# Optimization experiments

Measured on AMD Instinct MI355X. Metric: run time of the kernel, lower is better.

## Reference

```python
import jax, jax.numpy as jnp
import numpy as np

N = 10000      # nodes
E = 160000     # edges (before self-loops)
IN = 256
NEG_SLOPE = 0.2  # PyG GATConv default


def gat_layer(x, src, dst, W, a_src, a_dst, bias, heads, concat, n):
    # x: [n, in_dim]; W: [in_dim, heads*C]; a_src/a_dst: [heads, C]
    C = W.shape[1] // heads
    h = (x @ W).reshape(n, heads, C)                      # [n,H,C]
    es = jnp.einsum('nhc,hc->nh', h, a_src)               # [n,H]
    ed = jnp.einsum('nhc,hc->nh', h, a_dst)               # [n,H]
    e = jax.nn.leaky_relu(es[src] + ed[dst], NEG_SLOPE)   # [E,H]
    # segment softmax over destination node (every node has a self-loop)
    emax = jax.ops.segment_max(e, dst, num_segments=n)    # [n,H]
    al = jnp.exp(e - emax[dst])                           # [E,H]
    den = jax.ops.segment_sum(al, dst, num_segments=n)    # [n,H]
    al = al / den[dst]
    out = jax.ops.segment_sum(h[src] * al[:, :, None], dst, num_segments=n)  # [n,H,C]
    out = out.reshape(n, heads * C) if concat else out.mean(axis=1)
    return out + bias


def setup_inputs() -> dict:
    key = jax.random.key(0)
    ks = jax.random.split(key, 16)
    s = 0.05
    p = lambda k, shp: jax.random.normal(k, shp, dtype=jnp.float32) * s
    return {
        'x': jax.random.normal(ks[0], (N, IN), dtype=jnp.float32),
        'edge_index': jax.random.randint(ks[1], (2, E), 0, N, dtype=jnp.int64),
        'proj_w': p(ks[2], (IN, 512)), 'proj_b': jnp.zeros((512,), jnp.float32),
        'w1': p(ks[3], (512, 4 * 512)),  'as1': p(ks[4], (4, 512)), 'ad1': p(ks[5], (4, 512)),  'b1': jnp.zeros((2048,), jnp.float32),
        'w2': p(ks[6], (2048, 4 * 512)), 'as2': p(ks[7], (4, 512)), 'ad2': p(ks[8], (4, 512)),  'b2': jnp.zeros((2048,), jnp.float32),
        'w3': p(ks[9], (2048, 2 * 512)), 'as3': p(ks[10], (2, 512)), 'ad3': p(ks[11], (2, 512)), 'b3': jnp.zeros((512,), jnp.float32),
    }


def reference(x, edge_index, proj_w, proj_b, w1, as1, ad1, b1,
              w2, as2, ad2, b2, w3, as3, ad3, b3):
    n = x.shape[0]
    loops = jnp.arange(n, dtype=edge_index.dtype)
    src = jnp.concatenate([edge_index[0], loops])   # PyG add_self_loops=True
    dst = jnp.concatenate([edge_index[1], loops])
    h = x @ proj_w + proj_b                         # dropout is identity in eval
    h = gat_layer(h, src, dst, w1, as1, ad1, b1, 4, True, n)
    h = jax.nn.elu(h)
    h = gat_layer(h, src, dst, w2, as2, ad2, b2, 4, True, n)
    h = jax.nn.elu(h)
    h = gat_layer(h, src, dst, w3, as3, ad3, b3, 2, False, n)
    return h
```

## Files before the change

### kernel.cpp

```cpp
#include <hip/hip_runtime.h>
#include <hip/hip_bf16.h>
#include <math.h>

#define CDIV(a,b) (((a)+(b)-1)/(b))

typedef __bf16  bf16x8 __attribute__((ext_vector_type(8)));
typedef float   f32x4  __attribute__((ext_vector_type(4)));
typedef unsigned short u16x8 __attribute__((ext_vector_type(8)));
typedef unsigned short u16x4 __attribute__((ext_vector_type(4)));

__device__ __forceinline__ float bf2f(unsigned short u) {
    union { unsigned int i; float f; } x; x.i = ((unsigned int)u) << 16; return x.f;
}
__device__ __forceinline__ unsigned short f2bf(float f) {
    union { float f; unsigned int i; } x; x.f = f;
    unsigned int r = x.i + 0x7fff + ((x.i >> 16) & 1);
    return (unsigned short)(r >> 16);
}

__global__ void hist_kernel(const int* __restrict__ ei, int* __restrict__ deg,
                            int E, int Et) {
    int e = blockIdx.x * blockDim.x + threadIdx.x;
    if (e >= Et) return;
    int d = (e < E) ? ei[E + e] : (e - E);
    atomicAdd(&deg[d], 1);
}

__global__ void scan_kernel(const int* __restrict__ deg, int* __restrict__ off, int n) {
    __shared__ int wsum[16];
    __shared__ int carry_s;
    int t = threadIdx.x, lane = t & 63, wv = t >> 6;
    if (t == 0) carry_s = 0;
    __syncthreads();
    for (int base = 0; base < n; base += 1024) {
        int v = (base + t < n) ? deg[base + t] : 0;
        int x = v;
#pragma unroll
        for (int o = 1; o < 64; o <<= 1) {
            int y = __shfl_up(x, o);
            if (lane >= o) x += y;
        }
        if (lane == 63) wsum[wv] = x;
        __syncthreads();
        if (wv == 0 && lane < 16) {
            int s = wsum[lane];
#pragma unroll
            for (int o = 1; o < 16; o <<= 1) {
                int y = __shfl_up(s, o);
                if (lane >= o) s += y;
            }
            wsum[lane] = s;
        }
        __syncthreads();
        int wprev = (wv == 0) ? 0 : wsum[wv - 1];
        int incl = carry_s + wprev + x;
        if (base + t < n) off[base + t] = incl - v;
        __syncthreads();
        if (t == 1023) carry_s = incl;
        __syncthreads();
    }
    if (t == 0) off[n] = carry_s;
}

__global__ void scatter_kernel(const int* __restrict__ ei, const int* __restrict__ off,
                               int* __restrict__ cur, int* __restrict__ csr,
                               int E, int Et) {
    int e = blockIdx.x * blockDim.x + threadIdx.x;
    if (e >= Et) return;
    int s, d;
    if (e < E) { s = ei[e]; d = ei[E + e]; } else { s = e - E; d = s; }
    int pos = off[d] + atomicAdd(&cur[d], 1);
    csr[pos] = s;
}

__global__ void prep_t_kernel(const float* __restrict__ wa, __hip_bfloat16* __restrict__ wta,
                              const float* __restrict__ wb, __hip_bfloat16* __restrict__ wtb,
                              const float* __restrict__ wc, __hip_bfloat16* __restrict__ wtc,
                              int t0, int t1, int t2) {
    __shared__ float tile[32][33];
    int bid = blockIdx.x;
    const float* w; __hip_bfloat16* wt; int K, N, r;
    if (bid < t0)      { w = wa; wt = wta; K = 512;  N = 2048; r = bid; }
    else if (bid < t1) { w = wb; wt = wtb; K = 2048; N = 2048; r = bid - t0; }
    else               { w = wc; wt = wtc; K = 2048; N = 1024; r = bid - t1; }
    (void)t2;
    int kt = K >> 5;
    int kb = (r % kt) * 32, nb = (r / kt) * 32;
    int tx = threadIdx.x & 31, ty = threadIdx.x >> 5;
    for (int i = ty; i < 32; i += 8)
        tile[i][tx] = w[(size_t)(kb + i) * N + nb + tx];
    __syncthreads();
    for (int i = ty; i < 32; i += 8)
        wt[(size_t)(nb + i) * K + kb + tx] = __float2bfloat16(tile[tx][i]);
}

__global__ void cvt2_kernel(const float* __restrict__ a, __hip_bfloat16* __restrict__ ao,
                            int na4,
                            const float* __restrict__ b, __hip_bfloat16* __restrict__ bo,
                            int nb4) {
    int i = blockIdx.x * blockDim.x + threadIdx.x;
    const float* src; __hip_bfloat16* dst; int idx;
    if (i < na4) { src = a; dst = ao; idx = i * 4; }
    else if (i < na4 + nb4) { src = b; dst = bo; idx = (i - na4) * 4; }
    else return;
    float4 v = *(const float4*)(src + idx);
    dst[idx + 0] = __float2bfloat16(v.x);
    dst[idx + 1] = __float2bfloat16(v.y);
    dst[idx + 2] = __float2bfloat16(v.z);
    dst[idx + 3] = __float2bfloat16(v.w);
}

__global__ void beff_kernel(const float* __restrict__ pb, const float* __restrict__ w1,
                            float* __restrict__ beff, int N) {
    int j  = blockIdx.x * 256 + threadIdx.x;
    int k0 = blockIdx.y * 64;
    float s = 0.f;
#pragma unroll
    for (int k = 0; k < 64; k++)
        s = fmaf(pb[k0 + k], w1[(size_t)(k0 + k) * N + j], s);
    atomicAdd(&beff[j], s);
}

__global__ void va_kernel(const __hip_bfloat16* __restrict__ w_efft,
                          const float* __restrict__ b_eff,
                          const float* __restrict__ as1, const float* __restrict__ ad1,
                          const float* __restrict__ b1,
                          float* __restrict__ va, float* __restrict__ cvec,
                          float* __restrict__ b1s) {
    int j = blockIdx.x, t = threadIdx.x;
    if (j == 8) {
        for (int i = t; i < 2048; i += 256) b1s[i] = b_eff[i] + b1[i];
        return;
    }
    int h = j & 3;
    const float* a = ((j < 4) ? as1 : ad1) + h * 512;
    __shared__ float aLDS[512];
    __shared__ float red[256];
    for (int c = t; c < 512; c += 256) aLDS[c] = a[c];
    __syncthreads();
    float acc = 0.f;
    const unsigned short* wb = (const unsigned short*)w_efft + (size_t)h * 512 * 256 + t;
    for (int c = 0; c < 512; c++)
        acc = fmaf(aLDS[c], bf2f(wb[(size_t)c * 256]), acc);
    va[j * 256 + t] = acc;
    float cp = b_eff[h * 512 + t] * aLDS[t] + b_eff[h * 512 + 256 + t] * aLDS[256 + t];
    red[t] = cp;
    __syncthreads();
    for (int s = 128; s > 0; s >>= 1) {
        if (t < s) red[t] += red[t + s];
        __syncthreads();
    }
    if (t == 0) cvec[j] = red[0];
}

__global__ void es1_kernel(const __hip_bfloat16* __restrict__ x_bf,
                           const float* __restrict__ va, const float* __restrict__ cvec,
                           float* __restrict__ es, float* __restrict__ ed) {
    int node = blockIdx.x, l = threadIdx.x;
    u16x4 xv = *(const u16x4*)((const unsigned short*)x_bf + (size_t)node * 256 + l * 4);
    float xf[4];
#pragma unroll
    for (int k = 0; k < 4; k++) xf[k] = bf2f(xv[k]);
    float dot[8];
#pragma unroll
    for (int j = 0; j < 8; j++) {
        float4 v = *(const float4*)(va + j * 256 + l * 4);
        dot[j] = xf[0] * v.x + xf[1] * v.y + xf[2] * v.z + xf[3] * v.w;
    }
#pragma unroll
    for (int j = 0; j < 8; j++)
        for (int o = 32; o; o >>= 1) dot[j] += __shfl_down(dot[j], o);
    if (l == 0) {
#pragma unroll
        for (int h = 0; h < 4; h++) {
            es[node * 4 + h] = dot[h] + cvec[h];
            ed[node * 4 + h] = dot[4 + h] + cvec[4 + h];
        }
    }
}

__global__ __launch_bounds__(256) void agg1x_kernel(
    const __hip_bfloat16* __restrict__ x_bf, const float* __restrict__ es,
    const float* __restrict__ ed, const int* __restrict__ csr,
    const int* __restrict__ off, __hip_bfloat16* __restrict__ z)
{
    __shared__ float alds[64][4];
    __shared__ int   slds[64];
    int d = blockIdx.x, t = threadIdx.x;
    int beg = off[d], end = off[d + 1];
    float acc[4] = {0.f, 0.f, 0.f, 0.f}, den[4] = {0.f, 0.f, 0.f, 0.f};
    float edd[4];
#pragma unroll
    for (int h = 0; h < 4; h++) edd[h] = ed[d * 4 + h];
    const unsigned short* xb = (const unsigned short*)x_bf;

    for (int cb = beg; cb < end; cb += 64) {
        int cl = end - cb; if (cl > 64) cl = 64;
        int i = t >> 2, h = t & 3;
        if (i < cl) {
            int s = csr[cb + i];
            if (h == 0) slds[i] = s;
            float e = es[s * 4 + h] + edd[h];
            e = (e > 0.f) ? e : 0.2f * e;
            alds[i][h] = __expf(e);
        }
        __syncthreads();
        for (int ii = 0; ii < cl; ii++) {
            int s = slds[ii];
            float xv = bf2f(xb[(size_t)s * 256 + t]);
#pragma unroll
            for (int hh = 0; hh < 4; hh++) {
                float a = alds[ii][hh];
                den[hh] += a;
                acc[hh] = fmaf(a, xv, acc[hh]);
            }
        }
        __syncthreads();
    }
    unsigned short* zb = (unsigned short*)z + (size_t)d * 1024;
#pragma unroll
    for (int h = 0; h < 4; h++)
        zb[h * 256 + t] = f2bf(acc[h] / den[h]);
}

__device__ __forceinline__ void gload16(void* lds, const void* g) {
    __builtin_amdgcn_global_load_lds(
        (const __attribute__((address_space(1))) void*)g,
        (__attribute__((address_space(3))) void*)lds, 16, 0, 0);
}

__global__ __launch_bounds__(256) void gemm_bf16_kernel(
    const __hip_bfloat16* __restrict__ A,
    const __hip_bfloat16* __restrict__ BT,
    const float* __restrict__ bias,
    __hip_bfloat16* __restrict__ Cb,
    int M, int N, int K, int lda, int hko, int do_elu,
    int MB, int NB, int XT, int NBH)
{
    __shared__ __align__(16) __hip_bfloat16 As[128 * 32];
    __shared__ __align__(16) __hip_bfloat16 Bs[128 * 32];

    const int bid  = blockIdx.x;
    const int xcd  = bid & 7;
    const int slot = bid >> 3;
    const int per_yh = XT * NBH;
    const int yh    = slot / per_yh;
    const int rem   = slot - yh * per_yh;
    const int x_sub = rem / NBH;
    const int ys    = rem - x_sub * NBH;
    const int yb    = yh * NBH + ys;
    const int xb    = xcd * XT + x_sub;
    if (xb >= MB || yb >= NB) return;

    const int tid = threadIdx.x;
    const int m0 = xb * 128, n0 = yb * 128;
    const int w = tid >> 6, l = tid & 63;
    const int wm = (w & 1) * 64, wn = (w >> 1) * 64;
    const int lm = l & 15, lq = l >> 4;

    f32x4 acc[4][4] = {};

    const int arow = tid >> 2;
    const int acol = (tid & 3) * 8;
    const __hip_bfloat16* Ag = A + (size_t)(m0 + arow) * lda + acol + (n0 >> 9) * hko;
    const __hip_bfloat16* Bg = BT + (size_t)(n0 + arow) * K + acol;
    char* AsW = (char*)As + (w << 10);
    char* BsW = (char*)Bs + (w << 10);

    for (int k0 = 0; k0 < K; k0 += 32) {
        gload16(AsW,        Ag + k0);
        gload16(AsW + 4096, Ag + (size_t)64 * lda + k0);
        gload16(BsW,        Bg + k0);
        gload16(BsW + 4096, Bg + (size_t)64 * K + k0);
        __syncthreads();
        bf16x8 af[4], bfr[4];
#pragma unroll
        for (int i = 0; i < 4; i++)
            af[i] = *(const bf16x8*)(As + (wm + i * 16 + lm) * 32 + lq * 8);
#pragma unroll
        for (int j = 0; j < 4; j++)
            bfr[j] = *(const bf16x8*)(Bs + (wn + j * 16 + lm) * 32 + lq * 8);
#pragma unroll
        for (int i = 0; i < 4; i++)
#pragma unroll
            for (int j = 0; j < 4; j++)
                acc[i][j] = __builtin_amdgcn_mfma_f32_16x16x32_bf16(
                    af[i], bfr[j], acc[i][j], 0, 0, 0);
        __syncthreads();
    }

#pragma unroll
    for (int i = 0; i < 4; i++) {
        int rb = m0 + wm + i * 16 + lq * 4;
#pragma unroll
        for (int r = 0; r < 4; r++) {
            int row = rb + r;
            if (row >= M) continue;
#pragma unroll
            for (int j = 0; j < 4; j++) {
                int col = n0 + wn + j * 16 + lm;
                float v = acc[i][j][r];
                if (bias) v += bias[col];
                if (do_elu) v = (v > 0.f) ? v : expm1f(v);
                Cb[(size_t)row * N + col] = __float2bfloat16(v);
            }
        }
    }
}

__global__ __launch_bounds__(512, 2) void gemm256_kernel(
    const __hip_bfloat16* __restrict__ A,
    const __hip_bfloat16* __restrict__ BT,
    __hip_bfloat16* __restrict__ Cb,
    int M, int N, int K, int MT, int nfull)
{
    __shared__ __align__(16) char smem[131072];
    const int NT = K >> 6;

    const int cpx  = gridDim.x >> 3;
    const int bid  = blockIdx.x;
    const int slot = (bid & 7) * cpx + (bid >> 3);
    int mt, ntl;
    if (slot < nfull) { mt = slot % MT; ntl = slot / MT; }
    else              { ntl = nfull / MT; mt = (nfull % MT) + (slot - nfull); }
    const int m0 = mt << 8, n0 = ntl << 8;

    const int tid = threadIdx.x;
    const int w  = tid >> 6, l = tid & 63;
    const int wr = w >> 2, wc = w & 3;
    const int lm = l & 15, lq = l >> 4;

    const int srow = tid >> 3;
    const int scol = ((l & 7) << 3) ^ ((l >> 3) << 3);
    const __hip_bfloat16* As0 = A  + (size_t)(m0 + srow) * K + scol;
    const __hip_bfloat16* Bs0 = BT + (size_t)(n0 + srow) * K + scol;
    const size_t rs64  = (size_t)64  * K;
    const size_t rs128 = (size_t)128 * K;
    char* const stA = smem +          ((size_t)w << 10);
    char* const stB = smem + 65536 +  ((size_t)w << 10);

    auto STAGE_A = [&](int par, int hf, int tt) {
        char* d = stA + (((par << 1) | hf) << 14);
        const __hip_bfloat16* s = As0 + (size_t)hf * rs128 + (tt << 6);
        gload16(d,        s);
        gload16(d + 8192, s + rs64);
    };
    auto STAGE_B = [&](int par, int hf, int tt) {
        char* d = stB + (((par << 1) | hf) << 14);
        const __hip_bfloat16* s = Bs0 + (size_t)hf * rs128 + (tt << 6);
        gload16(d,        s);
        gload16(d + 8192, s + rs64);
    };

    const int roff = lm << 7;
    const int xm   = (lm & 7) << 4;
    const int off0 = (lq << 4) ^ xm;
    const int off1 = off0 ^ 64;
    const int bsel = 65536 + ((wc & 1) << 13);

    f32x4  acc[8][4] = {};
    bf16x8 af[8][2];
    bf16x8 bfr[2][2];

    STAGE_A(0, 0, 0); STAGE_A(0, 1, 0);
    STAGE_B(0, 0, 0); STAGE_B(0, 1, 0);
    STAGE_A(1, 0, 1); STAGE_A(1, 1, 1);
    asm volatile("s_waitcnt vmcnt(4)" ::: "memory");
    __builtin_amdgcn_s_barrier();

    for (int t = 0; t < NT; ++t) {
        const int par = t & 1;
        const char* aS = smem + (((par << 1) | wr)        << 14) + roff;
        const char* bS = smem + (((par << 1) | (wc >> 1)) << 14) + bsel + roff;

#pragma unroll
        for (int i = 0; i < 4; ++i) {
            af[i][0] = *(const bf16x8*)(aS + i * 2048 + off0);
            af[i][1] = *(const bf16x8*)(aS + i * 2048 + off1);
        }
#pragma unroll
        for (int j = 0; j < 2; ++j) {
            bfr[j][0] = *(const bf16x8*)(bS + j * 2048 + off0);
            bfr[j][1] = *(const bf16x8*)(bS + j * 2048 + off1);
        }
        if (t + 1 < NT) STAGE_B(par ^ 1, 0, t + 1);
        __builtin_amdgcn_s_barrier();
        asm volatile("s_waitcnt lgkmcnt(0)" ::: "memory");
        __builtin_amdgcn_sched_barrier(0);
        __builtin_amdgcn_s_setprio(1);
#pragma unroll
        for (int i = 0; i < 4; ++i)
#pragma unroll
            for (int j = 0; j < 2; ++j) {
                acc[i][j] = __builtin_amdgcn_mfma_f32_16x16x32_bf16(af[i][0], bfr[j][0], acc[i][j], 0, 0, 0);
                acc[i][j] = __builtin_amdgcn_mfma_f32_16x16x32_bf16(af[i][1], bfr[j][1], acc[i][j], 0, 0, 0);
            }
        __builtin_amdgcn_s_setprio(0);
        __builtin_amdgcn_s_barrier();

#pragma unroll
        for (int i = 4; i < 8; ++i) {
            af[i][0] = *(const bf16x8*)(aS + i * 2048 + off0);
            af[i][1] = *(const bf16x8*)(aS + i * 2048 + off1);
        }
        if (t + 1 < NT) STAGE_B(par ^ 1, 1, t + 1);
        __builtin_amdgcn_s_barrier();
        asm volatile("s_waitcnt lgkmcnt(0)" ::: "memory");
        __builtin_amdgcn_sched_barrier(0);
        __builtin_amdgcn_s_setprio(1);
#pragma unroll
        for (int i = 4; i < 8; ++i)
#pragma unroll
            for (int j = 0; j < 2; ++j) {
                acc[i][j] = __builtin_amdgcn_mfma_f32_16x16x32_bf16(af[i][0], bfr[j][0], acc[i][j], 0, 0, 0);
                acc[i][j] = __builtin_amdgcn_mfma_f32_16x16x32_bf16(af[i][1], bfr[j][1], acc[i][j], 0, 0, 0);
            }
        __builtin_amdgcn_s_setprio(0);
        __builtin_amdgcn_s_barrier();

#pragma unroll
        for (int j = 0; j < 2; ++j) {
            bfr[j][0] = *(const bf16x8*)(bS + (j + 2) * 2048 + off0);
            bfr[j][1] = *(const bf16x8*)(bS + (j + 2) * 2048 + off1);
        }
        if (t + 2 < NT) STAGE_A(par, 0, t + 2);
        __builtin_amdgcn_s_barrier();
        asm volatile("s_waitcnt lgkmcnt(0)" ::: "memory");
        __builtin_amdgcn_sched_barrier(0);
        __builtin_amdgcn_s_setprio(1);
#pragma unroll
        for (int i = 0; i < 4; ++i)
#pragma unroll
            for (int j = 0; j < 2; ++j) {
                acc[i][j + 2] = __builtin_amdgcn_mfma_f32_16x16x32_bf16(af[i][0], bfr[j][0], acc[i][j + 2], 0, 0, 0);
                acc[i][j + 2] = __builtin_amdgcn_mfma_f32_16x16x32_bf16(af[i][1], bfr[j][1], acc[i][j + 2], 0, 0, 0);
            }
        __builtin_amdgcn_s_setprio(0);
        __builtin_amdgcn_s_barrier();

        if (t + 2 < NT) STAGE_A(par, 1, t + 2);
        __builtin_amdgcn_s_barrier();
        __builtin_amdgcn_sched_barrier(0);
        __builtin_amdgcn_s_setprio(1);
#pragma unroll
        for (int i = 4; i < 8; ++i)
#pragma unroll
            for (int j = 0; j < 2; ++j) {
                acc[i][j + 2] = __builtin_amdgcn_mfma_f32_16x16x32_bf16(af[i][0], bfr[j][0], acc[i][j + 2], 0, 0, 0);
                acc[i][j + 2] = __builtin_amdgcn_mfma_f32_16x16x32_bf16(af[i][1], bfr[j][1], acc[i][j + 2], 0, 0, 0);
            }
        __builtin_amdgcn_s_setprio(0);
        if (t + 2 < NT)      { asm volatile("s_waitcnt vmcnt(4)" ::: "memory"); }
        else if (t + 1 < NT) { asm volatile("s_waitcnt vmcnt(0)" ::: "memory"); }
        __builtin_amdgcn_s_barrier();
    }

#pragma unroll
    for (int i = 0; i < 8; ++i) {
        int rb = m0 + wr * 128 + i * 16 + lq * 4;
#pragma unroll
        for (int r = 0; r < 4; ++r) {
            int row = rb + r;
            if (row >= M) continue;
#pragma unroll
            for (int j = 0; j < 4; ++j) {
                int col = n0 + wc * 64 + j * 16 + lm;
                Cb[(size_t)row * N + col] = __float2bfloat16(acc[i][j][r]);
            }
        }
    }
}

__global__ __launch_bounds__(256, 2) void gemm128_kernel(
    const __hip_bfloat16* __restrict__ A,
    const __hip_bfloat16* __restrict__ BT,
    __hip_bfloat16* __restrict__ Cb,
    int M, int N, int K, int mode, int RT)
{
    __shared__ __align__(16) char smem[65536];
    const int NT = K >> 6;

    const int cpx  = gridDim.x >> 3;
    const int bid  = blockIdx.x;
    const int slot = (bid & 7) * cpx + (bid >> 3);
    int r, c;
    if (mode == 0) { r = slot % RT; c = slot / RT; }
    else {
        if (slot < 96) { c = 12 + slot / 48; r = 32 + slot % 48; }
        else           { int u = slot - 96; c = 14 + u / 80; r = u % 80; }
    }
    const int m0 = r << 7, n0 = c << 7;

    const int tid = threadIdx.x;
    const int w = tid >> 6, l = tid & 63;
    const int wm = (w & 1) << 6, wn = (w >> 1) << 6;
    const int lm = l & 15, lq = l >> 4;

    const int srow = tid >> 3;
    const int scol = (((tid & 7) ^ ((tid >> 3) & 7)) << 3);
    const __hip_bfloat16* Ag = A  + (size_t)(m0 + srow) * K + scol;
    const __hip_bfloat16* Bg = BT + (size_t)(n0 + srow) * K + scol;
    const size_t rs32 = (size_t)32 * K;
    char* const dA = smem +         ((size_t)w << 10);
    char* const dB = smem + 16384 + ((size_t)w << 10);

    auto STAGE = [&](int par, int tt) {
        char* pa = dA + (par << 15);
        char* pb = dB + (par << 15);
        const __hip_bfloat16* sa = Ag + (tt << 6);
        const __hip_bfloat16* sb = Bg + (tt << 6);
#pragma unroll
        for (int s = 0; s < 4; ++s) {
            gload16(pa + (s << 12), sa + (size_t)s * rs32);
            gload16(pb + (s << 12), sb + (size_t)s * rs32);
        }
    };

    const int roff = lm << 7;
    const int off0 = (lq << 4) ^ ((lm & 7) << 4);
    const int off1 = off0 ^ 64;

    f32x4 acc[4][4] = {};

    STAGE(0, 0);
    asm volatile("s_waitcnt vmcnt(0)" ::: "memory");
    __builtin_amdgcn_s_barrier();

    for (int t = 0; t < NT; ++t) {
        const int par = t & 1;
        if (t + 1 < NT) STAGE(par ^ 1, t + 1);
        const char* aS = smem + (par << 15) +         wm * 128 + roff;
        const char* bS = smem + (par << 15) + 16384 + wn * 128 + roff;
        bf16x8 af[4][2], bfr[4][2];
#pragma unroll
        for (int i = 0; i < 4; ++i) {
            af[i][0]  = *(const bf16x8*)(aS + i * 2048 + off0);
            af[i][1]  = *(const bf16x8*)(aS + i * 2048 + off1);
            bfr[i][0] = *(const bf16x8*)(bS + i * 2048 + off0);
            bfr[i][1] = *(const bf16x8*)(bS + i * 2048 + off1);
        }
        asm volatile("s_waitcnt lgkmcnt(0)" ::: "memory");
        __builtin_amdgcn_sched_barrier(0);
        __builtin_amdgcn_s_setprio(1);
#pragma unroll
        for (int i = 0; i < 4; ++i)
#pragma unroll
            for (int j = 0; j < 4; ++j) {
                acc[i][j] = __builtin_amdgcn_mfma_f32_16x16x32_bf16(af[i][0], bfr[j][0], acc[i][j], 0, 0, 0);
                acc[i][j] = __builtin_amdgcn_mfma_f32_16x16x32_bf16(af[i][1], bfr[j][1], acc[i][j], 0, 0, 0);
            }
        __builtin_amdgcn_s_setprio(0);
        if (t + 1 < NT) asm volatile("s_waitcnt vmcnt(0)" ::: "memory");
        __builtin_amdgcn_s_barrier();
    }

#pragma unroll
    for (int i = 0; i < 4; ++i) {
        int rb = m0 + wm + i * 16 + lq * 4;
#pragma unroll
        for (int r2 = 0; r2 < 4; ++r2) {
            int row = rb + r2;
            if (row >= M) continue;
#pragma unroll
            for (int j = 0; j < 4; ++j) {
                int col = n0 + wn + j * 16 + lm;
                Cb[(size_t)row * N + col] = __float2bfloat16(acc[i][j][r2]);
            }
        }
    }
}

__global__ void esed_kernel(const __hip_bfloat16* __restrict__ h,
                            const float* __restrict__ a_src,
                            const float* __restrict__ a_dst,
                            float* __restrict__ es, float* __restrict__ ed, int H) {
    int nidx = blockIdx.x;
    int t = threadIdx.x;
    int head = t >> 6, lane = t & 63;
    const unsigned short* hp =
        (const unsigned short*)h + (size_t)nidx * H * 512 + head * 512 + lane * 8;
    const float* sp = a_src + head * 512 + lane * 8;
    const float* dp = a_dst + head * 512 + lane * 8;
    u16x8 hv = *(const u16x8*)hp;
    float4 s0 = *(const float4*)sp, s1 = *(const float4*)(sp + 4);
    float4 d0 = *(const float4*)dp, d1 = *(const float4*)(dp + 4);
    float hf[8];
#pragma unroll
    for (int k = 0; k < 8; k++) hf[k] = bf2f(hv[k]);
    float s = hf[0]*s0.x + hf[1]*s0.y + hf[2]*s0.z + hf[3]*s0.w
            + hf[4]*s1.x + hf[5]*s1.y + hf[6]*s1.z + hf[7]*s1.w;
    float d = hf[0]*d0.x + hf[1]*d0.y + hf[2]*d0.z + hf[3]*d0.w
            + hf[4]*d1.x + hf[5]*d1.y + hf[6]*d1.z + hf[7]*d1.w;
    for (int o = 32; o; o >>= 1) { s += __shfl_down(s, o); d += __shfl_down(d, o); }
    if (lane == 0) { es[nidx * H + head] = s; ed[nidx * H + head] = d; }
}

template<int H, int VEC, bool MEAN>
__global__ __launch_bounds__(256) void agg_kernel(
    const __hip_bfloat16* __restrict__ h, const float* __restrict__ es,
    const float* __restrict__ ed, const int* __restrict__ csr,
    const int* __restrict__ off, const float* __restrict__ bias,
    float* __restrict__ outF, __hip_bfloat16* __restrict__ outB, int do_elu)
{
    constexpr int HS = H * 512;
    __shared__ float red[MEAN ? 1024 : 1];
    int d = blockIdx.x, t = threadIdx.x;
    int c0 = t * VEC;
    int head = c0 >> 9;
    float edd = ed[d * H + head];
    int beg = off[d], end = off[d + 1];
    float acc[VEC];
#pragma unroll
    for (int k = 0; k < VEC; k++) acc[k] = 0.f;
    float den = 0.f;
    const unsigned short* hb = (const unsigned short*)h;

    int i = beg;
    for (; i + 3 < end; i += 4) {
        int   s[4];
        float wgt[4];
#pragma unroll
        for (int u = 0; u < 4; u++) {
            s[u] = csr[i + u];
            float e = es[s[u] * H + head] + edd;
            e = (e > 0.f) ? e : 0.2f * e;
            wgt[u] = __expf(e);
        }
        if constexpr (VEC == 8) {
            u16x8 v[4];
#pragma unroll
            for (int u = 0; u < 4; u++)
                v[u] = *(const u16x8*)(hb + (size_t)s[u] * HS + c0);
#pragma unroll
            for (int u = 0; u < 4; u++) {
                den += wgt[u];
#pragma unroll
                for (int k = 0; k < 8; k++) acc[k] = fmaf(wgt[u], bf2f(v[u][k]), acc[k]);
            }
        } else {
            u16x4 v[4];
#pragma unroll
            for (int u = 0; u < 4; u++)
                v[u] = *(const u16x4*)(hb + (size_t)s[u] * HS + c0);
#pragma unroll
            for (int u = 0; u < 4; u++) {
                den += wgt[u];
#pragma unroll
                for (int k = 0; k < VEC; k++) acc[k] = fmaf(wgt[u], bf2f(v[u][k]), acc[k]);
            }
        }
    }
    for (; i < end; i++) {
        int s0 = csr[i];
        float e0 = es[s0 * H + head] + edd;
        e0 = (e0 > 0.f) ? e0 : 0.2f * e0;
        float w0 = __expf(e0);
        den += w0;
        const unsigned short* hp0 = hb + (size_t)s0 * HS + c0;
        if constexpr (VEC == 8) {
            u16x8 v0 = *(const u16x8*)hp0;
#pragma unroll
            for (int k = 0; k < 8; k++) acc[k] = fmaf(w0, bf2f(v0[k]), acc[k]);
        } else {
            u16x4 v0 = *(const u16x4*)hp0;
#pragma unroll
            for (int k = 0; k < VEC; k++) acc[k] = fmaf(w0, bf2f(v0[k]), acc[k]);
        }
    }

    float inv = 1.f / den;
    if constexpr (!MEAN) {
        u16x8 ov;
#pragma unroll
        for (int k = 0; k < VEC; k++) {
            float v = acc[k] * inv + bias[c0 + k];
            if (do_elu) v = (v > 0.f) ? v : expm1f(v);
            ov[k] = f2bf(v);
        }
        *(u16x8*)((unsigned short*)outB + (size_t)d * HS + c0) = ov;
    } else {
#pragma unroll
        for (int k = 0; k < VEC; k++) red[c0 + k] = acc[k] * inv;
        __syncthreads();
        if (t < 128) {
#pragma unroll
            for (int k = 0; k < 4; k++) {
                int c = t * 4 + k;
                outF[(size_t)d * 512 + c] = 0.5f * (red[c] + red[c + 512]) + bias[c];
            }
        }
    }
}

extern "C" void kernel_launch(void* const* d_in, const int* in_sizes, int n_in,
                              void* d_out, int out_size, void* d_ws, size_t ws_size,
                              hipStream_t stream) {
    const float* x      = (const float*)d_in[0];
    const int*   ei     = (const int*)  d_in[1];
    const float* proj_w = (const float*)d_in[2];
    const float* proj_b = (const float*)d_in[3];
    const float* w1  = (const float*)d_in[4];
    const float* as1 = (const float*)d_in[5];
    const float* ad1 = (const float*)d_in[6];
    const float* b1  = (const float*)d_in[7];
    const float* w2  = (const float*)d_in[8];
    const float* as2 = (const float*)d_in[9];
    const float* ad2 = (const float*)d_in[10];
    const float* b2  = (const float*)d_in[11];
    const float* w3  = (const float*)d_in[12];
    const float* as3 = (const float*)d_in[13];
    const float* ad3 = (const float*)d_in[14];
    const float* b3  = (const float*)d_in[15];

    const int n    = in_sizes[0] / 256;
    const int E    = in_sizes[1] / 2;
    const int Et   = E + n;
    const int MB   = CDIV(n, 128);
    const int MB2  = CDIV(n, 256);
    const int Mpad = MB2 * 256;
    const int XT   = CDIV(MB, 8);

    char* p = (char*)d_ws;
    auto carve = [&](size_t bytes) {
        void* r = (void*)p;
        p += (bytes + 255) & ~(size_t)255;
        return r;
    };
    __hip_bfloat16* h_bf    = (__hip_bfloat16*)carve((size_t)Mpad * 2048 * sizeof(__hip_bfloat16));
    __hip_bfloat16* act_bf  = (__hip_bfloat16*)carve((size_t)Mpad * 2048 * sizeof(__hip_bfloat16));
    __hip_bfloat16* x_bf    = (__hip_bfloat16*)carve((size_t)Mpad * 256 * sizeof(__hip_bfloat16));
    __hip_bfloat16* pw_bf   = (__hip_bfloat16*)carve((size_t)256 * 512 * sizeof(__hip_bfloat16));
    __hip_bfloat16* w1t     = (__hip_bfloat16*)carve((size_t)2048 * 512 * sizeof(__hip_bfloat16));
    __hip_bfloat16* w2t     = (__hip_bfloat16*)carve((size_t)2048 * 2048 * sizeof(__hip_bfloat16));
    __hip_bfloat16* w3t     = (__hip_bfloat16*)carve((size_t)1024 * 2048 * sizeof(__hip_bfloat16));
    __hip_bfloat16* w_efft  = (__hip_bfloat16*)carve((size_t)2048 * 256 * sizeof(__hip_bfloat16));
    float* b_eff = (float*)carve((size_t)2048 * sizeof(float));
    float* b1s   = (float*)carve((size_t)2048 * sizeof(float));
    float* va    = (float*)carve((size_t)8 * 256 * sizeof(float));
    float* cvec  = (float*)carve((size_t)8 * sizeof(float));
    float* es  = (float*)carve((size_t)n * 4 * sizeof(float));
    float* ed  = (float*)carve((size_t)n * 4 * sizeof(float));
    int* deg = (int*)carve((size_t)2 * n * sizeof(int));
    int* cur = deg + n;
    int* off = (int*)carve((size_t)(n + 1) * sizeof(int));
    int* csr = (int*)carve((size_t)Et * sizeof(int));
    __hip_bfloat16* z_bf = h_bf;
    (void)ws_size; (void)n_in;

    hipMemsetAsync(deg, 0, 2 * n * sizeof(int), stream);
    hipMemsetAsync(b_eff, 0, 2048 * sizeof(float), stream);
    hist_kernel<<<CDIV(Et, 256), 256, 0, stream>>>(ei, deg, E, Et);
    scan_kernel<<<1, 1024, 0, stream>>>(deg, off, n);
    scatter_kernel<<<CDIV(Et, 256), 256, 0, stream>>>(ei, off, cur, csr, E, Et);

    const int t0 = (512 / 32) * (2048 / 32);
    const int t1 = t0 + (2048 / 32) * (2048 / 32);
    const int t2 = t1 + (2048 / 32) * (1024 / 32);
    prep_t_kernel<<<t2, 256, 0, stream>>>(w1, w1t, w2, w2t, w3, w3t, t0, t1, t2);
    const int na4 = 256 * 512 / 4, nb4 = n * 256 / 4;
    cvt2_kernel<<<CDIV(na4 + nb4, 256), 256, 0, stream>>>(proj_w, pw_bf, na4, x, x_bf, nb4);

    gemm_bf16_kernel<<<8 * 2 * 2, 256, 0, stream>>>(
        w1t, pw_bf, nullptr, w_efft, 2048, 256, 512, 512, 0, 0, 16, 2, 2, 2);
    beff_kernel<<<dim3(2048 / 256, 512 / 64), 256, 0, stream>>>(proj_b, w1, b_eff, 2048);

    va_kernel<<<9, 256, 0, stream>>>(w_efft, b_eff, as1, ad1, b1, va, cvec, b1s);

    es1_kernel<<<n, 64, 0, stream>>>(x_bf, va, cvec, es, ed);
    agg1x_kernel<<<n, 256, 0, stream>>>(x_bf, es, ed, csr, off, z_bf);
    gemm_bf16_kernel<<<8 * XT * 16, 256, 0, stream>>>(
        z_bf, w_efft, b1s, act_bf, n, 2048, 256, 1024, 256, 1, MB, 16, XT, 16);

    gemm256_kernel<<<256, 512, 0, stream>>>(act_bf, w2t, h_bf, n, 2048, 2048, 40, 240);
    gemm128_kernel<<<256, 256, 0, stream>>>(act_bf, w2t, h_bf, n, 2048, 2048, 1, 0);
    esed_kernel<<<n, 4 * 64, 0, stream>>>(h_bf, as2, ad2, es, ed, 4);
    agg_kernel<4, 8, false><<<n, 256, 0, stream>>>(h_bf, es, ed, csr, off, b2,
                                                   nullptr, act_bf, 1);

    gemm128_kernel<<<640, 256, 0, stream>>>(act_bf, w3t, h_bf, n, 1024, 2048, 0, 80);
    esed_kernel<<<n, 2 * 64, 0, stream>>>(h_bf, as3, ad3, es, ed, 2);
    agg_kernel<2, 4, true><<<n, 256, 0, stream>>>(h_bf, es, ed, csr, off, b3,
                                                  (float*)d_out, nullptr, 0);
}
```

Baseline: 602.7 us.

## Split GAT aggregation into alpha precompute and XCD-sliced column aggregation

Replaces the per-destination-node aggregation kernels for layers 2 and 3 with a separate kernel that computes normalized attention coefficients per edge, followed by aggregation kernels. In those kernels each block owns one 256-column feature slice and walks many destination nodes, with the block index mapped so that each XCD works on a fixed slice. The aim is to keep each XCD's slice of the gathered h rows resident in its L2 and to drop the repeated exp and softmax work across threads. The costs are an extra alpha buffer, extra launches, and for layer 3 a float partial buffer plus a separate combine kernel to average the heads.

```diff
diff --git a/kernel.cpp b/kernel.cpp
--- a/kernel.cpp
+++ b/kernel.cpp
@@ -595,101 +595,156 @@
     if (lane == 0) { es[nidx * H + head] = s; ed[nidx * H + head] = d; }
 }
 
-template<int H, int VEC, bool MEAN>
-__global__ __launch_bounds__(256) void agg_kernel(
-    const __hip_bfloat16* __restrict__ h, const float* __restrict__ es,
-    const float* __restrict__ ed, const int* __restrict__ csr,
-    const int* __restrict__ off, const float* __restrict__ bias,
-    float* __restrict__ outF, __hip_bfloat16* __restrict__ outB, int do_elu)
+template<int H>
+__global__ __launch_bounds__(256) void alpha_kernel(
+    const float* __restrict__ es, const float* __restrict__ ed,
+    const int* __restrict__ csr, const int* __restrict__ off,
+    float* __restrict__ alpha, int n)
 {
-    constexpr int HS = H * 512;
-    __shared__ float red[MEAN ? 1024 : 1];
-    int d = blockIdx.x, t = threadIdx.x;
-    int c0 = t * VEC;
-    int head = c0 >> 9;
-    float edd = ed[d * H + head];
+    int d = blockIdx.x * 4 + (threadIdx.x >> 6);
+    if (d >= n) return;
+    int lane = threadIdx.x & 63;
     int beg = off[d], end = off[d + 1];
-    float acc[VEC];
-#pragma unroll
-    for (int k = 0; k < VEC; k++) acc[k] = 0.f;
-    float den = 0.f;
+    float edd[H], den[H];
+#pragma unroll
+    for (int h = 0; h < H; h++) { edd[h] = ed[d * H + h]; den[h] = 0.f; }
+    for (int i = beg + lane; i < end; i += 64) {
+        int s = csr[i];
+#pragma unroll
+        for (int h = 0; h < H; h++) {
+            float e = es[s * H + h] + edd[h];
+            e = (e > 0.f) ? e : 0.2f * e;
+            den[h] += __expf(e);
+        }
+    }
+#pragma unroll
+    for (int h = 0; h < H; h++) {
+        for (int o = 32; o; o >>= 1) den[h] += __shfl_down(den[h], o);
+        den[h] = __shfl(den[h], 0);
+        den[h] = 1.f / den[h];
+    }
+    for (int i = beg + lane; i < end; i += 64) {
+        int s = csr[i];
+#pragma unroll
+        for (int h = 0; h < H; h++) {
+            float e = es[s * H + h] + edd[h];
+            e = (e > 0.f) ? e : 0.2f * e;
+            alpha[(size_t)i * H + h] = __expf(e) * den[h];
+        }
+    }
+}
+
+__global__ __launch_bounds__(256) void agg2s_kernel(
+    const __hip_bfloat16* __restrict__ h, const float* __restrict__ alpha,
+    const int* __restrict__ csr, const int* __restrict__ off,
+    const float* __restrict__ bias, __hip_bfloat16* __restrict__ outB, int n)
+{
+    const int bid   = blockIdx.x;
+    const int slice = bid & 7;
+    const int head  = slice >> 1;
+    const int ws    = (bid >> 3) * 4 + (threadIdx.x >> 6);
+    const int lane  = threadIdx.x & 63;
+    const int c0    = slice * 256 + lane * 4;
     const unsigned short* hb = (const unsigned short*)h;
-
-    int i = beg;
-    for (; i + 3 < end; i += 4) {
-        int   s[4];
-        float wgt[4];
-#pragma unroll
-        for (int u = 0; u < 4; u++) {
-            s[u] = csr[i + u];
-            float e = es[s[u] * H + head] + edd;
-            e = (e > 0.f) ? e : 0.2f * e;
-            wgt[u] = __expf(e);
-        }
-        if constexpr (VEC == 8) {
-            u16x8 v[4];
-#pragma unroll
-            for (int u = 0; u < 4; u++)
-                v[u] = *(const u16x8*)(hb + (size_t)s[u] * HS + c0);
+    float b[4];
+#pragma unroll
+    for (int k = 0; k < 4; k++) b[k] = bias[c0 + k];
+
+    for (int d = ws; d < n; d += 512) {
+        int beg = off[d], end = off[d + 1];
+        float acc[4] = {0.f, 0.f, 0.f, 0.f};
+        int i = beg;
+        for (; i + 3 < end; i += 4) {
+            int sidx[4]; float a[4];
 #pragma unroll
             for (int u = 0; u < 4; u++) {
-                den += wgt[u];
-#pragma unroll
-                for (int k = 0; k < 8; k++) acc[k] = fmaf(wgt[u], bf2f(v[u][k]), acc[k]);
-            }
-        } else {
-            u16x4 v[4];
-#pragma unroll
-            for (int u = 0; u < 4; u++)
-                v[u] = *(const u16x4*)(hb + (size_t)s[u] * HS + c0);
+                sidx[u] = csr[i + u];
+                a[u] = alpha[(size_t)(i + u) * 4 + head];
+            }
 #pragma unroll
             for (int u = 0; u < 4; u++) {
-                den += wgt[u];
-#pragma unroll
-                for (int k = 0; k < VEC; k++) acc[k] = fmaf(wgt[u], bf2f(v[u][k]), acc[k]);
-            }
-        }
-    }
-    for (; i < end; i++) {
-        int s0 = csr[i];
-        float e0 = es[s0 * H + head] + edd;
-        e0 = (e0 > 0.f) ? e0 : 0.2f * e0;
-        float w0 = __expf(e0);
-        den += w0;
-        const unsigned short* hp0 = hb + (size_t)s0 * HS + c0;
-        if constexpr (VEC == 8) {
-            u16x8 v0 = *(const u16x8*)hp0;
-#pragma unroll
-            for (int k = 0; k < 8; k++) acc[k] = fmaf(w0, bf2f(v0[k]), acc[k]);
-        } else {
-            u16x4 v0 = *(const u16x4*)hp0;
-#pragma unroll
-            for (int k = 0; k < VEC; k++) acc[k] = fmaf(w0, bf2f(v0[k]), acc[k]);
-        }
-    }
-
-    float inv = 1.f / den;
-    if constexpr (!MEAN) {
-        u16x8 ov;
-#pragma unroll
-        for (int k = 0; k < VEC; k++) {
-            float v = acc[k] * inv + bias[c0 + k];
-            if (do_elu) v = (v > 0.f) ? v : expm1f(v);
+                u16x4 v = *(const u16x4*)(hb + (size_t)sidx[u] * 2048 + c0);
+#pragma unroll
+                for (int k = 0; k < 4; k++) acc[k] = fmaf(a[u], bf2f(v[k]), acc[k]);
+            }
+        }
+        for (; i < end; i++) {
+            int s = csr[i];
+            float a = alpha[(size_t)i * 4 + head];
+            u16x4 v = *(const u16x4*)(hb + (size_t)s * 2048 + c0);
+#pragma unroll
+            for (int k = 0; k < 4; k++) acc[k] = fmaf(a, bf2f(v[k]), acc[k]);
+        }
+        u16x4 ov;
+#pragma unroll
+        for (int k = 0; k < 4; k++) {
+            float v = acc[k] + b[k];
+            v = (v > 0.f) ? v : expm1f(v);
             ov[k] = f2bf(v);
         }
-        *(u16x8*)((unsigned short*)outB + (size_t)d * HS + c0) = ov;
-    } else {
-#pragma unroll
-        for (int k = 0; k < VEC; k++) red[c0 + k] = acc[k] * inv;
-        __syncthreads();
-        if (t < 128) {
-#pragma unroll
-            for (int k = 0; k < 4; k++) {
-                int c = t * 4 + k;
-                outF[(size_t)d * 512 + c] = 0.5f * (red[c] + red[c + 512]) + bias[c];
-            }
-        }
-    }
+        *(u16x4*)((unsigned short*)outB + (size_t)d * 2048 + c0) = ov;
+    }
+}
+
+__global__ __launch_bounds__(256) void agg3s_kernel(
+    const __hip_bfloat16* __restrict__ h, const float* __restrict__ alpha,
+    const int* __restrict__ csr, const int* __restrict__ off,
+    float* __restrict__ part, int n)
+{
+    const int bid   = blockIdx.x;
+    const int xcd   = bid & 7;
+    const int slice = xcd >> 1;
+    const int head  = slice >> 1;
+    const int ws    = (((bid >> 3) << 1) | (xcd & 1)) * 4 + (threadIdx.x >> 6);
+    const int lane  = threadIdx.x & 63;
+    const int c0    = slice * 256 + lane * 4;
+    const unsigned short* hb = (const unsigned short*)h;
+
+    for (int d = ws; d < n; d += 1024) {
+        int beg = off[d], end = off[d + 1];
+        float acc[4] = {0.f, 0.f, 0.f, 0.f};
+        int i = beg;
+        for (; i + 3 < end; i += 4) {
+            int sidx[4]; float a[4];
+#pragma unroll
+            for (int u = 0; u < 4; u++) {
+                sidx[u] = csr[i + u];
+                a[u] = alpha[(size_t)(i + u) * 2 + head];
+            }
+#pragma unroll
+            for (int u = 0; u < 4; u++) {
+                u16x4 v = *(const u16x4*)(hb + (size_t)sidx[u] * 1024 + c0);
+#pragma unroll
+                for (int k = 0; k < 4; k++) acc[k] = fmaf(a[u], bf2f(v[k]), acc[k]);
+            }
+        }
+        for (; i < end; i++) {
+            int s = csr[i];
+            float a = alpha[(size_t)i * 2 + head];
+            u16x4 v = *(const u16x4*)(hb + (size_t)s * 1024 + c0);
+#pragma unroll
+            for (int k = 0; k < 4; k++) acc[k] = fmaf(a, bf2f(v[k]), acc[k]);
+        }
+        *(float4*)(part + (size_t)d * 1024 + c0) =
+            make_float4(acc[0], acc[1], acc[2], acc[3]);
+    }
+}
+
+__global__ void comb3_kernel(const float* __restrict__ part,
+                             const float* __restrict__ b3,
+                             float* __restrict__ out, int n) {
+    int idx = blockIdx.x * 256 + threadIdx.x;
+    if (idx >= n * 128) return;
+    int d = idx >> 7, c = (idx & 127) * 4;
+    float4 p0 = *(const float4*)(part + (size_t)d * 1024 + c);
+    float4 p1 = *(const float4*)(part + (size_t)d * 1024 + 512 + c);
+    float4 bb = *(const float4*)(b3 + c);
+    float4 o;
+    o.x = 0.5f * (p0.x + p1.x) + bb.x;
+    o.y = 0.5f * (p0.y + p1.y) + bb.y;
+    o.z = 0.5f * (p0.z + p1.z) + bb.z;
+    o.w = 0.5f * (p0.w + p1.w) + bb.w;
+    *(float4*)(out + (size_t)d * 512 + c) = o;
 }
 
 extern "C" void kernel_launch(void* const* d_in, const int* in_sizes, int n_in,
@@ -740,11 +795,13 @@
     float* cvec  = (float*)carve((size_t)8 * sizeof(float));
     float* es  = (float*)carve((size_t)n * 4 * sizeof(float));
     float* ed  = (float*)carve((size_t)n * 4 * sizeof(float));
+    float* alpha = (float*)carve((size_t)Et * 4 * sizeof(float));
     int* deg = (int*)carve((size_t)2 * n * sizeof(int));
     int* cur = deg + n;
     int* off = (int*)carve((size_t)(n + 1) * sizeof(int));
     int* csr = (int*)carve((size_t)Et * sizeof(int));
     __hip_bfloat16* z_bf = h_bf;
+    float* part = (float*)act_bf;
     (void)ws_size; (void)n_in;
 
     hipMemsetAsync(deg, 0, 2 * n * sizeof(int), stream);
@@ -774,11 +831,12 @@
     gemm256_kernel<<<256, 512, 0, stream>>>(act_bf, w2t, h_bf, n, 2048, 2048, 40, 240);
     gemm128_kernel<<<256, 256, 0, stream>>>(act_bf, w2t, h_bf, n, 2048, 2048, 1, 0);
     esed_kernel<<<n, 4 * 64, 0, stream>>>(h_bf, as2, ad2, es, ed, 4);
-    agg_kernel<4, 8, false><<<n, 256, 0, stream>>>(h_bf, es, ed, csr, off, b2,
-                                                   nullptr, act_bf, 1);
+    alpha_kernel<4><<<CDIV(n, 4), 256, 0, stream>>>(es, ed, csr, off, alpha, n);
+    agg2s_kernel<<<1024, 256, 0, stream>>>(h_bf, alpha, csr, off, b2, act_bf, n);
 
     gemm128_kernel<<<640, 256, 0, stream>>>(act_bf, w3t, h_bf, n, 1024, 2048, 0, 80);
     esed_kernel<<<n, 2 * 64, 0, stream>>>(h_bf, as3, ad3, es, ed, 2);
-    agg_kernel<2, 4, true><<<n, 256, 0, stream>>>(h_bf, es, ed, csr, off, b3,
-                                                  (float*)d_out, nullptr, 0);
-}
+    alpha_kernel<2><<<CDIV(n, 4), 256, 0, stream>>>(es, ed, csr, off, alpha, n);
+    agg3s_kernel<<<1024, 256, 0, stream>>>(h_bf, alpha, csr, off, part, n);
+    comb3_kernel<<<CDIV(n * 128, 256), 256, 0, stream>>>(part, b3, (float*)d_out, n);
+}
```

Result: slower. 635.6 us (+5.5%).
